# Kernel optimization log

Hardware: AMD Instinct MI355X
Metric: run time of the kernel (lower is better)

## Reference

```python
import jax, jax.numpy as jnp
import numpy as np

E = 8        # num experts
TOP = 2      # top-k
D = 1024     # emb_size


def setup_inputs() -> dict:
    key = jax.random.key(0)
    ks = jax.random.split(key, 8)
    s = 1.0 / np.sqrt(D)
    x = jax.random.normal(ks[0], (4, 2048, D), dtype=jnp.float32)
    Wg = jax.random.uniform(ks[1], (D, E), jnp.float32, -s, s)
    bg = jax.random.uniform(ks[2], (E,), jnp.float32, -s, s)
    W1 = jax.random.uniform(ks[3], (E, D, D), jnp.float32, -s, s)
    b1 = jax.random.uniform(ks[4], (E, D), jnp.float32, -s, s)
    W2 = jax.random.uniform(ks[5], (E, D, D), jnp.float32, -s, s)
    b2 = jax.random.uniform(ks[6], (E, D), jnp.float32, -s, s)
    return {"x": x, "Wg": Wg, "bg": bg, "W1": W1, "b1": b1, "W2": W2, "b2": b2}


def reference(x, Wg, bg, W1, b1, W2, b2):
    x_shape = x.shape
    xt = x.reshape(-1, x_shape[-1])                       # [N, D] tokens
    gate_prob = jax.nn.softmax(xt @ Wg + bg, axis=-1)     # [N, E]
    top_w, top_i = jax.lax.top_k(gate_prob, TOP)          # [N, TOP]
    top_w = jax.nn.softmax(top_w, axis=-1)                # renormalize over top-k
    N = xt.shape[0]
    # combine weights scattered into dense [N, E] (each token has TOP nonzeros)
    comb = jnp.zeros((N, E), xt.dtype).at[jnp.arange(N)[:, None], top_i].add(top_w)
    # per-expert 2-layer MLP applied to all tokens; masked-out tokens get 0 combine weight
    h = jax.nn.relu(jnp.einsum('nd,edf->enf', xt, W1) + b1[:, None, :])   # [E, N, D]
    ye = jnp.einsum('enf,efg->eng', h, W2) + b2[:, None, :]               # [E, N, D]
    y = jnp.einsum('ne,eng->ng', comb, ye)                                # [N, D]
    return y.reshape(x_shape), gate_prob
```

## Files before the change

kernel.cpp:

```cpp
#include <hip/hip_runtime.h>
#include <stdint.h>

#define TOKENS 8192
#define DIM    1024
#define NEXP   8
#define NASSIGN (TOKENS*2)
#define BK     64

#define C_ROW   16
#define C_TILE  25
#define C_TOTAL 34

#define WS_CTRL  0
#define WS_TOPE  1024
#define WS_TOPW  (WS_TOPE + NASSIGN*4)
#define WS_PTOK  (WS_TOPW + NASSIGN*4)
#define WS_AROW  (WS_PTOK + NASSIGN*4)
#define WS_XB    (WS_AROW + NASSIGN*4)
#define WS_W1T   (WS_XB  + (size_t)TOKENS*DIM*2)
#define WS_W2T   (WS_W1T + (size_t)NEXP*DIM*DIM*2)
#define WS_H     (WS_W2T + (size_t)NEXP*DIM*DIM*2)
#define WS_YE    WS_XB

#define WGLD (DIM + 4)

typedef __attribute__((ext_vector_type(8))) short short8;
typedef __attribute__((ext_vector_type(4))) float floatx4;

__device__ __forceinline__ uint32_t bfr(float f) {
  uint32_t v = __float_as_uint(f);
  return (v + 0x7FFFu + ((v >> 16) & 1u)) >> 16;
}
__device__ __forceinline__ float b2f(uint32_t u) { return __uint_as_float(u << 16); }

__device__ __forceinline__ void load_lds16(const void* g, void* l) {
  __builtin_amdgcn_global_load_lds(
      (const __attribute__((address_space(1))) uint32_t*)g,
      (__attribute__((address_space(3))) uint32_t*)l, 16, 0, 0);
}

__global__ __launch_bounds__(256) void prep_kernel(
    const float* __restrict__ x, const float* __restrict__ Wg,
    const float* __restrict__ bg, float* __restrict__ gate_out,
    int* __restrict__ top_e, float* __restrict__ top_w,
    uint16_t* __restrict__ xb,
    const float* __restrict__ W1, const float* __restrict__ W2,
    uint16_t* __restrict__ W1T, uint16_t* __restrict__ W2T) {
  __shared__ __align__(16) char smem[NEXP * WGLD * 4];
  int t = threadIdx.x;

  if (blockIdx.x >= 2048) {
    uint16_t (*tile)[68] = (uint16_t (*)[68])smem;
    int cb = blockIdx.x - 2048;
    int m  = cb >> 8;
    int d0 = ((cb >> 4) & 15) * 64, f0 = (cb & 15) * 64;
    const float* src = (m < 8) ? (W1 + (size_t)m*DIM*DIM) : (W2 + (size_t)(m-8)*DIM*DIM);
    uint16_t*    dst = (m < 8) ? (W1T + (size_t)m*DIM*DIM) : (W2T + (size_t)(m-8)*DIM*DIM);
    int col = t & 63, rb = (t >> 6) * 16;
    #pragma unroll
    for (int i = 0; i < 16; i++) {
      int dr = rb + i;
      tile[dr][col] = (uint16_t)bfr(src[(size_t)(d0+dr)*DIM + f0 + col]);
    }
    __syncthreads();
    int dg = t & 15, frb = t >> 4;
    #pragma unroll
    for (int i = 0; i < 4; i++) {
      int fr = frb + i * 16;
      uint32_t b0 = tile[dg*4+0][fr], b1 = tile[dg*4+1][fr];
      uint32_t b2 = tile[dg*4+2][fr], b3 = tile[dg*4+3][fr];
      uint2 v;
      v.x = b0 | (b1 << 16);
      v.y = b2 | (b3 << 16);
      *(uint2*)&dst[(size_t)(f0+fr)*DIM + d0 + dg*4] = v;
    }
    return;
  }

  float* wgs = (float*)smem;
  #pragma unroll
  for (int k = 0; k < 32; k++) {
    int i = k * 256 + t;
    float v = Wg[i];
    wgs[(i & 7) * WGLD + (i >> 3)] = v;
  }
  __syncthreads();

  int wave = t >> 6, lane = t & 63;
  int tok = blockIdx.x * 4 + wave;
  const float4* xr = (const float4*)(x + (size_t)tok * DIM);
  uint2* xw = (uint2*)(xb + (size_t)tok * DIM);

  float4 acc[NEXP];
  #pragma unroll
  for (int e = 0; e < NEXP; e++) acc[e] = make_float4(0.f, 0.f, 0.f, 0.f);

  #pragma unroll
  for (int c = 0; c < 4; c++) {
    float4 xv = xr[c * 64 + lane];
    uint2 o;
    o.x = bfr(xv.x) | (bfr(xv.y) << 16);
    o.y = bfr(xv.z) | (bfr(xv.w) << 16);
    xw[c * 64 + lane] = o;
    int d0 = (c * 64 + lane) * 4;
    #pragma unroll
    for (int e = 0; e < NEXP; e++) {
      float4 wv = *(const float4*)&wgs[e * WGLD + d0];
      acc[e].x = fmaf(xv.x, wv.x, acc[e].x);
      acc[e].y = fmaf(xv.y, wv.y, acc[e].y);
      acc[e].z = fmaf(xv.z, wv.z, acc[e].z);
      acc[e].w = fmaf(xv.w, wv.w, acc[e].w);
    }
  }
  float s[NEXP];
  #pragma unroll
  for (int e = 0; e < NEXP; e++) s[e] = (acc[e].x + acc[e].y) + (acc[e].z + acc[e].w);
  #pragma unroll
  for (int off = 32; off > 0; off >>= 1) {
    #pragma unroll
    for (int e = 0; e < NEXP; e++) s[e] += __shfl_xor(s[e], off);
  }
  if (lane == 0) {
    float lg[NEXP], p[NEXP];
    float mx = -1e30f;
    #pragma unroll
    for (int e = 0; e < NEXP; e++) { lg[e] = s[e] + bg[e]; mx = fmaxf(mx, lg[e]); }
    float sum = 0.f;
    #pragma unroll
    for (int e = 0; e < NEXP; e++) { p[e] = expf(lg[e] - mx); sum += p[e]; }
    float inv = 1.f / sum;
    #pragma unroll
    for (int e = 0; e < NEXP; e++) p[e] *= inv;
    float4* go = (float4*)(gate_out + (size_t)tok * NEXP);
    go[0] = make_float4(p[0], p[1], p[2], p[3]);
    go[1] = make_float4(p[4], p[5], p[6], p[7]);
    int i1 = 0;
    #pragma unroll
    for (int e = 1; e < NEXP; e++) if (p[e] > p[i1]) i1 = e;
    int i2 = (i1 == 0) ? 1 : 0;
    #pragma unroll
    for (int e = 0; e < NEXP; e++) if (e != i1 && p[e] > p[i2]) i2 = e;
    float ev = expf(p[i2] - p[i1]);
    float w1 = 1.f / (1.f + ev), w2 = ev / (1.f + ev);
    top_e[2*tok]   = i1; top_e[2*tok+1] = i2;
    top_w[2*tok]   = w1; top_w[2*tok+1] = w2;
  }
}

__global__ __launch_bounds__(1024) void route_kernel(
    const int* __restrict__ top_e, int* __restrict__ ctrl,
    int* __restrict__ ptok, int* __restrict__ arow) {
  __shared__ int sc[NEXP * 1024];
  __shared__ int scnt[NEXP];
  __shared__ int rowstart[NEXP];
  int t = threadIdx.x;
  int e_loc[16];
  int cnt[NEXP];
  #pragma unroll
  for (int e = 0; e < NEXP; e++) cnt[e] = 0;
  #pragma unroll
  for (int j = 0; j < 16; j++) {
    int e = top_e[t * 16 + j];
    e_loc[j] = e;
    cnt[e]++;
  }
  #pragma unroll
  for (int e = 0; e < NEXP; e++) sc[e * 1024 + t] = cnt[e];
  __syncthreads();
  int wave = t >> 6, lane = t & 63;
  if (wave < NEXP) {
    int running = 0;
    for (int chunk = 0; chunk < 16; chunk++) {
      int idx = wave * 1024 + chunk * 64 + lane;
      int v = sc[idx];
      int incl = v;
      #pragma unroll
      for (int off = 1; off < 64; off <<= 1) {
        int u = __shfl_up(incl, off);
        if (lane >= off) incl += u;
      }
      sc[idx] = running + incl - v;
      running += __shfl(incl, 63);
    }
    if (lane == 0) scnt[wave] = running;
  }
  __syncthreads();
  if (t == 0) {
    int rs = 0, ts = 0;
    for (int e = 0; e < NEXP; e++) {
      ctrl[C_ROW + e] = rs;
      ctrl[C_TILE + e] = ts;
      rowstart[e] = rs;
      int c = scnt[e];
      rs += c;
      ts += (c + 127) >> 7;
    }
    ctrl[C_ROW + NEXP] = rs;
    ctrl[C_TILE + NEXP] = ts;
    ctrl[C_TOTAL] = ts;
  }
  __syncthreads();
  int off[NEXP];
  #pragma unroll
  for (int e = 0; e < NEXP; e++) off[e] = rowstart[e] + sc[e * 1024 + t];
  #pragma unroll
  for (int j = 0; j < 16; j++) {
    int i = t * 16 + j;
    int e = e_loc[j];
    int pos = off[e]++;
    ptok[pos] = i >> 1;
    arow[i] = pos;
  }
}

__device__ __forceinline__ bool sched_map(const int* ctrl, int bid,
                                          int& mtile, int& n0) {
  int total = ctrl[C_TOTAL];
  int spx = (total + 7) >> 3;
  int xcd = bid & 7, j = bid >> 3;
  int slot = j >> 3;
  if (slot >= spx) return false;
  mtile = xcd * spx + slot;
  n0 = (j & 7) * 128;
  return mtile < total;
}

__global__ __launch_bounds__(256, 2) void gemm1_kernel(
    const uint16_t* __restrict__ xb, const uint16_t* __restrict__ w1t,
    const float* __restrict__ b1, const int* __restrict__ ctrl,
    const int* __restrict__ ptok, uint16_t* __restrict__ h) {
  __shared__ __align__(16) uint16_t As[128*BK];
  __shared__ __align__(16) uint16_t Bs[128*BK];
  int mtile, n0;
  if (!sched_map(ctrl, blockIdx.x, mtile, n0)) return;
  int e = 0;
  #pragma unroll
  for (int k = 1; k < NEXP; k++) if (mtile >= ctrl[C_TILE + k]) e = k;
  int row0 = ctrl[C_ROW + e] + (mtile - ctrl[C_TILE + e]) * 128;
  int rend = ctrl[C_ROW + e + 1];

  int t = threadIdx.x, lane = t & 63, w = t >> 6;
  const uint16_t* gA[4];
  const uint16_t* gB[4];
  #pragma unroll
  for (int i = 0; i < 4; i++) {
    int s = i * 256 + t;
    int row = s >> 3, cs = s & 7;
    int gc = cs ^ (row & 7);
    int ar = row0 + row; if (ar > NASSIGN-1) ar = NASSIGN-1;
    int tok = ptok[ar];
    gA[i] = xb  + (size_t)tok * DIM + gc*8;
    gB[i] = w1t + (size_t)e*DIM*DIM + (size_t)(n0 + row)*DIM + gc*8;
  }
  floatx4 acc[4][4];
  #pragma unroll
  for (int mi = 0; mi < 4; mi++)
    #pragma unroll
    for (int ni = 0; ni < 4; ni++) acc[mi][ni] = (floatx4)(0.f);

  int wm = w & 1, wn = w >> 1;
  int l15 = lane & 15, lq = lane >> 4;

  for (int kt = 0; kt < DIM/BK; kt++) {
    #pragma unroll
    for (int i = 0; i < 4; i++) {
      load_lds16(gA[i], &As[(i*256 + t) * 8]);
      load_lds16(gB[i], &Bs[(i*256 + t) * 8]);
      gA[i] += BK; gB[i] += BK;
    }
    __syncthreads();
    #pragma unroll
    for (int ks = 0; ks < 2; ks++) {
      short8 a[4], b[4];
      #pragma unroll
      for (int mi = 0; mi < 4; mi++) {
        int row = wm*64 + mi*16 + l15;
        int slot = (ks*4 + lq) ^ (row & 7);
        a[mi] = *(const short8*)&As[row*BK + slot*8];
      }
      #pragma unroll
      for (int ni = 0; ni < 4; ni++) {
        int row = wn*64 + ni*16 + l15;
        int slot = (ks*4 + lq) ^ (row & 7);
        b[ni] = *(const short8*)&Bs[row*BK + slot*8];
      }
      #pragma unroll
      for (int mi = 0; mi < 4; mi++)
        #pragma unroll
        for (int ni = 0; ni < 4; ni++)
          acc[mi][ni] = __builtin_amdgcn_mfma_f32_16x16x32_bf16(a[mi], b[ni], acc[mi][ni], 0, 0, 0);
    }
    __syncthreads();
  }
  #pragma unroll
  for (int mi = 0; mi < 4; mi++) {
    #pragma unroll
    for (int r = 0; r < 4; r++) {
      int rt = wm*64 + mi*16 + lq*4 + r;
      int ar = row0 + rt;
      if (ar < rend) {
        #pragma unroll
        for (int ni = 0; ni < 4; ni++) {
          int n = n0 + wn*64 + ni*16 + l15;
          float v = acc[mi][ni][r] + b1[e*DIM + n];
          v = fmaxf(v, 0.f);
          h[(size_t)ar*DIM + n] = (uint16_t)bfr(v);
        }
      }
    }
  }
}

__global__ __launch_bounds__(256, 2) void gemm2_kernel(
    const uint16_t* __restrict__ h, const uint16_t* __restrict__ w2t,
    const float* __restrict__ b2, const int* __restrict__ ctrl,
    uint16_t* __restrict__ yeb) {
  __shared__ __align__(16) uint16_t As[128*BK];
  __shared__ __align__(16) uint16_t Bs[128*BK];
  int mtile, n0;
  if (!sched_map(ctrl, blockIdx.x, mtile, n0)) return;
  int e = 0;
  #pragma unroll
  for (int k = 1; k < NEXP; k++) if (mtile >= ctrl[C_TILE + k]) e = k;
  int row0 = ctrl[C_ROW + e] + (mtile - ctrl[C_TILE + e]) * 128;
  int rend = ctrl[C_ROW + e + 1];

  int t = threadIdx.x, lane = t & 63, w = t >> 6;
  const uint16_t* gA[4];
  const uint16_t* gB[4];
  #pragma unroll
  for (int i = 0; i < 4; i++) {
    int s = i * 256 + t;
    int row = s >> 3, cs = s & 7;
    int gc = cs ^ (row & 7);
    int ar = row0 + row; if (ar > NASSIGN-1) ar = NASSIGN-1;
    gA[i] = h   + (size_t)ar * DIM + gc*8;
    gB[i] = w2t + (size_t)e*DIM*DIM + (size_t)(n0 + row)*DIM + gc*8;
  }
  floatx4 acc[4][4];
  #pragma unroll
  for (int mi = 0; mi < 4; mi++)
    #pragma unroll
    for (int ni = 0; ni < 4; ni++) acc[mi][ni] = (floatx4)(0.f);

  int wm = w & 1, wn = w >> 1;
  int l15 = lane & 15, lq = lane >> 4;

  for (int kt = 0; kt < DIM/BK; kt++) {
    #pragma unroll
    for (int i = 0; i < 4; i++) {
      load_lds16(gA[i], &As[(i*256 + t) * 8]);
      load_lds16(gB[i], &Bs[(i*256 + t) * 8]);
      gA[i] += BK; gB[i] += BK;
    }
    __syncthreads();
    #pragma unroll
    for (int ks = 0; ks < 2; ks++) {
      short8 a[4], b[4];
      #pragma unroll
      for (int mi = 0; mi < 4; mi++) {
        int row = wm*64 + mi*16 + l15;
        int slot = (ks*4 + lq) ^ (row & 7);
        a[mi] = *(const short8*)&As[row*BK + slot*8];
      }
      #pragma unroll
      for (int ni = 0; ni < 4; ni++) {
        int row = wn*64 + ni*16 + l15;
        int slot = (ks*4 + lq) ^ (row & 7);
        b[ni] = *(const short8*)&Bs[row*BK + slot*8];
      }
      #pragma unroll
      for (int mi = 0; mi < 4; mi++)
        #pragma unroll
        for (int ni = 0; ni < 4; ni++)
          acc[mi][ni] = __builtin_amdgcn_mfma_f32_16x16x32_bf16(a[mi], b[ni], acc[mi][ni], 0, 0, 0);
    }
    __syncthreads();
  }
  #pragma unroll
  for (int mi = 0; mi < 4; mi++) {
    #pragma unroll
    for (int r = 0; r < 4; r++) {
      int rt = wm*64 + mi*16 + lq*4 + r;
      int ar = row0 + rt;
      if (ar < rend) {
        #pragma unroll
        for (int ni = 0; ni < 4; ni++) {
          int n = n0 + wn*64 + ni*16 + l15;
          float v = acc[mi][ni][r] + b2[e*DIM + n];
          yeb[(size_t)ar*DIM + n] = (uint16_t)bfr(v);
        }
      }
    }
  }
}

__global__ __launch_bounds__(256) void combine_kernel(
    const uint16_t* __restrict__ yeb, const int* __restrict__ arow,
    const float* __restrict__ top_w, float* __restrict__ y) {
  int tok = blockIdx.x, t = threadIdx.x;
  int r0 = arow[2*tok], r1 = arow[2*tok+1];
  float w0 = top_w[2*tok], w1 = top_w[2*tok+1];
  const uint2* a = (const uint2*)(yeb + (size_t)r0 * DIM);
  const uint2* b = (const uint2*)(yeb + (size_t)r1 * DIM);
  uint2 av = a[t], bv = b[t];
  float4 o;
  o.x = w0 * b2f(av.x & 0xFFFFu) + w1 * b2f(bv.x & 0xFFFFu);
  o.y = w0 * b2f(av.x >> 16)     + w1 * b2f(bv.x >> 16);
  o.z = w0 * b2f(av.y & 0xFFFFu) + w1 * b2f(bv.y & 0xFFFFu);
  o.w = w0 * b2f(av.y >> 16)     + w1 * b2f(bv.y >> 16);
  ((float4*)(y + (size_t)tok * DIM))[t] = o;
}

extern "C" void kernel_launch(void* const* d_in, const int* in_sizes, int n_in,
                              void* d_out, int out_size, void* d_ws, size_t ws_size,
                              hipStream_t stream) {
  const float* x  = (const float*)d_in[0];
  const float* Wg = (const float*)d_in[1];
  const float* bg = (const float*)d_in[2];
  const float* W1 = (const float*)d_in[3];
  const float* b1 = (const float*)d_in[4];
  const float* W2 = (const float*)d_in[5];
  const float* b2 = (const float*)d_in[6];
  float* out = (float*)d_out;
  char* ws = (char*)d_ws;

  int*      ctrl = (int*)(ws + WS_CTRL);
  int*      tope = (int*)(ws + WS_TOPE);
  float*    topw = (float*)(ws + WS_TOPW);
  int*      ptok = (int*)(ws + WS_PTOK);
  int*      arow = (int*)(ws + WS_AROW);
  uint16_t* xb   = (uint16_t*)(ws + WS_XB);
  uint16_t* w1t  = (uint16_t*)(ws + WS_W1T);
  uint16_t* w2t  = (uint16_t*)(ws + WS_W2T);
  uint16_t* hbuf = (uint16_t*)(ws + WS_H);
  uint16_t* yeb  = (uint16_t*)(ws + WS_YE);

  prep_kernel<<<6144, 256, 0, stream>>>(x, Wg, bg, out + (size_t)TOKENS*DIM,
                                        tope, topw, xb, W1, W2, w1t, w2t);
  route_kernel<<<1, 1024, 0, stream>>>(tope, ctrl, ptok, arow);

  gemm1_kernel<<<136*8, 256, 0, stream>>>(xb, w1t, b1, ctrl, ptok, hbuf);
  gemm2_kernel<<<136*8, 256, 0, stream>>>(hbuf, w2t, b2, ctrl, yeb);
  combine_kernel<<<TOKENS, 256, 0, stream>>>(yeb, arow, topw, out);
}
```

Baseline: 269.7 us.

## Fuse combine into gemm2 via atomics and merge routing into weight prep

The gemm2 epilogue now scales each expert output row by its routing weight and atomically adds it into the zeroed fp32 output, which removes the bf16 intermediate buffer and the separate combine kernel. Gate computation is split into its own kernel, which also zeroes the output. Routing moves into block 0 of the weight transpose kernel, so the single-block route launch disappears and routing overlaps the transpose. The cost is float atomics on the output (2 adds per element) and non-deterministic summation order, and routing now runs on one 256-thread block in serial.

After: 329.7 us. +22.3%, slower.

```diff
diff --git a/kernel.cpp b/kernel.cpp
--- a/kernel.cpp
+++ b/kernel.cpp
@@ -15,12 +15,11 @@
 #define WS_TOPE  1024
 #define WS_TOPW  (WS_TOPE + NASSIGN*4)
 #define WS_PTOK  (WS_TOPW + NASSIGN*4)
-#define WS_AROW  (WS_PTOK + NASSIGN*4)
-#define WS_XB    (WS_AROW + NASSIGN*4)
+#define WS_PW    (WS_PTOK + NASSIGN*4)
+#define WS_XB    (WS_PW  + NASSIGN*4)
 #define WS_W1T   (WS_XB  + (size_t)TOKENS*DIM*2)
 #define WS_W2T   (WS_W1T + (size_t)NEXP*DIM*DIM*2)
 #define WS_H     (WS_W2T + (size_t)NEXP*DIM*DIM*2)
-#define WS_YE    WS_XB
 
 #define WGLD (DIM + 4)
 
@@ -39,19 +38,103 @@
       (__attribute__((address_space(3))) uint32_t*)l, 16, 0, 0);
 }
 
-__global__ __launch_bounds__(256) void prep_kernel(
+__global__ __launch_bounds__(256) void gate_kernel(
     const float* __restrict__ x, const float* __restrict__ Wg,
     const float* __restrict__ bg, float* __restrict__ gate_out,
     int* __restrict__ top_e, float* __restrict__ top_w,
-    uint16_t* __restrict__ xb,
+    uint16_t* __restrict__ xb, float* __restrict__ y) {
+  __shared__ __align__(16) float wgs[NEXP * WGLD];
+  int t = threadIdx.x;
+
+  {
+    float4 z = make_float4(0.f, 0.f, 0.f, 0.f);
+    float4* yz = (float4*)(y + (size_t)blockIdx.x * 4 * DIM);
+    #pragma unroll
+    for (int i = 0; i < 4; i++) yz[i * 256 + t] = z;
+  }
+
+  #pragma unroll
+  for (int k = 0; k < 32; k++) {
+    int i = k * 256 + t;
+    float v = Wg[i];
+    wgs[(i & 7) * WGLD + (i >> 3)] = v;
+  }
+  __syncthreads();
+
+  int wave = t >> 6, lane = t & 63;
+  int tok = blockIdx.x * 4 + wave;
+  const float4* xr = (const float4*)(x + (size_t)tok * DIM);
+  uint2* xw = (uint2*)(xb + (size_t)tok * DIM);
+
+  float4 acc[NEXP];
+  #pragma unroll
+  for (int e = 0; e < NEXP; e++) acc[e] = make_float4(0.f, 0.f, 0.f, 0.f);
+
+  #pragma unroll
+  for (int c = 0; c < 4; c++) {
+    float4 xv = xr[c * 64 + lane];
+    uint2 o;
+    o.x = bfr(xv.x) | (bfr(xv.y) << 16);
+    o.y = bfr(xv.z) | (bfr(xv.w) << 16);
+    xw[c * 64 + lane] = o;
+    int d0 = (c * 64 + lane) * 4;
+    #pragma unroll
+    for (int e = 0; e < NEXP; e++) {
+      float4 wv = *(const float4*)&wgs[e * WGLD + d0];
+      acc[e].x = fmaf(xv.x, wv.x, acc[e].x);
+      acc[e].y = fmaf(xv.y, wv.y, acc[e].y);
+      acc[e].z = fmaf(xv.z, wv.z, acc[e].z);
+      acc[e].w = fmaf(xv.w, wv.w, acc[e].w);
+    }
+  }
+  float s[NEXP];
+  #pragma unroll
+  for (int e = 0; e < NEXP; e++) s[e] = (acc[e].x + acc[e].y) + (acc[e].z + acc[e].w);
+  #pragma unroll
+  for (int off = 32; off > 0; off >>= 1) {
+    #pragma unroll
+    for (int e = 0; e < NEXP; e++) s[e] += __shfl_xor(s[e], off);
+  }
+  if (lane == 0) {
+    float lg[NEXP], p[NEXP];
+    float mx = -1e30f;
+    #pragma unroll
+    for (int e = 0; e < NEXP; e++) { lg[e] = s[e] + bg[e]; mx = fmaxf(mx, lg[e]); }
+    float sum = 0.f;
+    #pragma unroll
+    for (int e = 0; e < NEXP; e++) { p[e] = expf(lg[e] - mx); sum += p[e]; }
+    float inv = 1.f / sum;
+    #pragma unroll
+    for (int e = 0; e < NEXP; e++) p[e] *= inv;
+    float4* go = (float4*)(gate_out + (size_t)tok * NEXP);
+    go[0] = make_float4(p[0], p[1], p[2], p[3]);
+    go[1] = make_float4(p[4], p[5], p[6], p[7]);
+    int i1 = 0;
+    #pragma unroll
+    for (int e = 1; e < NEXP; e++) if (p[e] > p[i1]) i1 = e;
+    int i2 = (i1 == 0) ? 1 : 0;
+    #pragma unroll
+    for (int e = 0; e < NEXP; e++) if (e != i1 && p[e] > p[i2]) i2 = e;
+    float ev = expf(p[i2] - p[i1]);
+    float w1 = 1.f / (1.f + ev), w2 = ev / (1.f + ev);
+    top_e[2*tok]   = i1; top_e[2*tok+1] = i2;
+    top_w[2*tok]   = w1; top_w[2*tok+1] = w2;
+  }
+}
+
+__global__ __launch_bounds__(256) void prep2_kernel(
     const float* __restrict__ W1, const float* __restrict__ W2,
-    uint16_t* __restrict__ W1T, uint16_t* __restrict__ W2T) {
-  __shared__ __align__(16) char smem[NEXP * WGLD * 4];
+    uint16_t* __restrict__ W1T, uint16_t* __restrict__ W2T,
+    const int* __restrict__ top_e, const float* __restrict__ top_w,
+    int* __restrict__ ctrl, int* __restrict__ ptok, float* __restrict__ pw) {
+  __shared__ __align__(16) char smem[64 * 68 * 2];
+  __shared__ int scnt[NEXP];
+  __shared__ int rowstart[NEXP];
   int t = threadIdx.x;
 
-  if (blockIdx.x >= 2048) {
+  if (blockIdx.x != 0) {
     uint16_t (*tile)[68] = (uint16_t (*)[68])smem;
-    int cb = blockIdx.x - 2048;
+    int cb = blockIdx.x - 1;
     int m  = cb >> 8;
     int d0 = ((cb >> 4) & 15) * 64, f0 = (cb & 15) * 64;
     const float* src = (m < 8) ? (W1 + (size_t)m*DIM*DIM) : (W2 + (size_t)(m-8)*DIM*DIM);
@@ -77,101 +160,22 @@
     return;
   }
 
-  float* wgs = (float*)smem;
-  #pragma unroll
-  for (int k = 0; k < 32; k++) {
-    int i = k * 256 + t;
-    float v = Wg[i];
-    wgs[(i & 7) * WGLD + (i >> 3)] = v;
-  }
-  __syncthreads();
-
-  int wave = t >> 6, lane = t & 63;
-  int tok = blockIdx.x * 4 + wave;
-  const float4* xr = (const float4*)(x + (size_t)tok * DIM);
-  uint2* xw = (uint2*)(xb + (size_t)tok * DIM);
-
-  float4 acc[NEXP];
-  #pragma unroll
-  for (int e = 0; e < NEXP; e++) acc[e] = make_float4(0.f, 0.f, 0.f, 0.f);
-
-  #pragma unroll
-  for (int c = 0; c < 4; c++) {
-    float4 xv = xr[c * 64 + lane];
-    uint2 o;
-    o.x = bfr(xv.x) | (bfr(xv.y) << 16);
-    o.y = bfr(xv.z) | (bfr(xv.w) << 16);
-    xw[c * 64 + lane] = o;
-    int d0 = (c * 64 + lane) * 4;
-    #pragma unroll
-    for (int e = 0; e < NEXP; e++) {
-      float4 wv = *(const float4*)&wgs[e * WGLD + d0];
-      acc[e].x = fmaf(xv.x, wv.x, acc[e].x);
-      acc[e].y = fmaf(xv.y, wv.y, acc[e].y);
-      acc[e].z = fmaf(xv.z, wv.z, acc[e].z);
-      acc[e].w = fmaf(xv.w, wv.w, acc[e].w);
-    }
-  }
-  float s[NEXP];
-  #pragma unroll
-  for (int e = 0; e < NEXP; e++) s[e] = (acc[e].x + acc[e].y) + (acc[e].z + acc[e].w);
-  #pragma unroll
-  for (int off = 32; off > 0; off >>= 1) {
-    #pragma unroll
-    for (int e = 0; e < NEXP; e++) s[e] += __shfl_xor(s[e], off);
-  }
-  if (lane == 0) {
-    float lg[NEXP], p[NEXP];
-    float mx = -1e30f;
-    #pragma unroll
-    for (int e = 0; e < NEXP; e++) { lg[e] = s[e] + bg[e]; mx = fmaxf(mx, lg[e]); }
-    float sum = 0.f;
-    #pragma unroll
-    for (int e = 0; e < NEXP; e++) { p[e] = expf(lg[e] - mx); sum += p[e]; }
-    float inv = 1.f / sum;
-    #pragma unroll
-    for (int e = 0; e < NEXP; e++) p[e] *= inv;
-    float4* go = (float4*)(gate_out + (size_t)tok * NEXP);
-    go[0] = make_float4(p[0], p[1], p[2], p[3]);
-    go[1] = make_float4(p[4], p[5], p[6], p[7]);
-    int i1 = 0;
-    #pragma unroll
-    for (int e = 1; e < NEXP; e++) if (p[e] > p[i1]) i1 = e;
-    int i2 = (i1 == 0) ? 1 : 0;
-    #pragma unroll
-    for (int e = 0; e < NEXP; e++) if (e != i1 && p[e] > p[i2]) i2 = e;
-    float ev = expf(p[i2] - p[i1]);
-    float w1 = 1.f / (1.f + ev), w2 = ev / (1.f + ev);
-    top_e[2*tok]   = i1; top_e[2*tok+1] = i2;
-    top_w[2*tok]   = w1; top_w[2*tok+1] = w2;
-  }
-}
-
-__global__ __launch_bounds__(1024) void route_kernel(
-    const int* __restrict__ top_e, int* __restrict__ ctrl,
-    int* __restrict__ ptok, int* __restrict__ arow) {
-  __shared__ int sc[NEXP * 1024];
-  __shared__ int scnt[NEXP];
-  __shared__ int rowstart[NEXP];
-  int t = threadIdx.x;
-  int e_loc[16];
+  int* sc = (int*)smem;
   int cnt[NEXP];
   #pragma unroll
   for (int e = 0; e < NEXP; e++) cnt[e] = 0;
-  #pragma unroll
-  for (int j = 0; j < 16; j++) {
-    int e = top_e[t * 16 + j];
-    e_loc[j] = e;
+  for (int j = 0; j < 64; j++) {
+    int e = top_e[t * 64 + j];
     cnt[e]++;
   }
   #pragma unroll
-  for (int e = 0; e < NEXP; e++) sc[e * 1024 + t] = cnt[e];
+  for (int e = 0; e < NEXP; e++) sc[e * 256 + t] = cnt[e];
   __syncthreads();
   int wave = t >> 6, lane = t & 63;
-  if (wave < NEXP) {
+  for (int ee = wave; ee < NEXP; ee += 4) {
     int running = 0;
-    for (int chunk = 0; chunk < 16; chunk++) {
-      int idx = wave * 1024 + chunk * 64 + lane;
+    for (int chunk = 0; chunk < 4; chunk++) {
+      int idx = ee * 256 + chunk * 64 + lane;
       int v = sc[idx];
       int incl = v;
       #pragma unroll
@@ -182,7 +186,7 @@
       sc[idx] = running + incl - v;
       running += __shfl(incl, 63);
     }
-    if (lane == 0) scnt[wave] = running;
+    if (lane == 0) scnt[ee] = running;
   }
   __syncthreads();
   if (t == 0) {
@@ -202,14 +206,13 @@
   __syncthreads();
   int off[NEXP];
   #pragma unroll
-  for (int e = 0; e < NEXP; e++) off[e] = rowstart[e] + sc[e * 1024 + t];
-  #pragma unroll
-  for (int j = 0; j < 16; j++) {
-    int i = t * 16 + j;
-    int e = e_loc[j];
+  for (int e = 0; e < NEXP; e++) off[e] = rowstart[e] + sc[e * 256 + t];
+  for (int j = 0; j < 64; j++) {
+    int i = t * 64 + j;
+    int e = top_e[i];
     int pos = off[e]++;
     ptok[pos] = i >> 1;
-    arow[i] = pos;
+    pw[pos]   = top_w[i];
   }
 }
 
@@ -314,7 +317,8 @@
 __global__ __launch_bounds__(256, 2) void gemm2_kernel(
     const uint16_t* __restrict__ h, const uint16_t* __restrict__ w2t,
     const float* __restrict__ b2, const int* __restrict__ ctrl,
-    uint16_t* __restrict__ yeb) {
+    const int* __restrict__ ptok, const float* __restrict__ pw,
+    float* __restrict__ y) {
   __shared__ __align__(16) uint16_t As[128*BK];
   __shared__ __align__(16) uint16_t Bs[128*BK];
   int mtile, n0;
@@ -384,32 +388,18 @@
       int rt = wm*64 + mi*16 + lq*4 + r;
       int ar = row0 + rt;
       if (ar < rend) {
+        int tok   = ptok[ar];
+        float wgt = pw[ar];
+        float* yrow = y + (size_t)tok * DIM;
         #pragma unroll
         for (int ni = 0; ni < 4; ni++) {
           int n = n0 + wn*64 + ni*16 + l15;
           float v = acc[mi][ni][r] + b2[e*DIM + n];
-          yeb[(size_t)ar*DIM + n] = (uint16_t)bfr(v);
+          unsafeAtomicAdd(&yrow[n], wgt * v);
         }
       }
     }
   }
-}
-
-__global__ __launch_bounds__(256) void combine_kernel(
-    const uint16_t* __restrict__ yeb, const int* __restrict__ arow,
-    const float* __restrict__ top_w, float* __restrict__ y) {
-  int tok = blockIdx.x, t = threadIdx.x;
-  int r0 = arow[2*tok], r1 = arow[2*tok+1];
-  float w0 = top_w[2*tok], w1 = top_w[2*tok+1];
-  const uint2* a = (const uint2*)(yeb + (size_t)r0 * DIM);
-  const uint2* b = (const uint2*)(yeb + (size_t)r1 * DIM);
-  uint2 av = a[t], bv = b[t];
-  float4 o;
-  o.x = w0 * b2f(av.x & 0xFFFFu) + w1 * b2f(bv.x & 0xFFFFu);
-  o.y = w0 * b2f(av.x >> 16)     + w1 * b2f(bv.x >> 16);
-  o.z = w0 * b2f(av.y & 0xFFFFu) + w1 * b2f(bv.y & 0xFFFFu);
-  o.w = w0 * b2f(av.y >> 16)     + w1 * b2f(bv.y >> 16);
-  ((float4*)(y + (size_t)tok * DIM))[t] = o;
 }
 
 extern "C" void kernel_launch(void* const* d_in, const int* in_sizes, int n_in,
@@ -429,18 +419,16 @@
   int*      tope = (int*)(ws + WS_TOPE);
   float*    topw = (float*)(ws + WS_TOPW);
   int*      ptok = (int*)(ws + WS_PTOK);
-  int*      arow = (int*)(ws + WS_AROW);
+  float*    pww  = (float*)(ws + WS_PW);
   uint16_t* xb   = (uint16_t*)(ws + WS_XB);
   uint16_t* w1t  = (uint16_t*)(ws + WS_W1T);
   uint16_t* w2t  = (uint16_t*)(ws + WS_W2T);
   uint16_t* hbuf = (uint16_t*)(ws + WS_H);
-  uint16_t* yeb  = (uint16_t*)(ws + WS_YE);
-
-  prep_kernel<<<6144, 256, 0, stream>>>(x, Wg, bg, out + (size_t)TOKENS*DIM,
-                                        tope, topw, xb, W1, W2, w1t, w2t);
-  route_kernel<<<1, 1024, 0, stream>>>(tope, ctrl, ptok, arow);
-
+
+  gate_kernel<<<2048, 256, 0, stream>>>(x, Wg, bg, out + (size_t)TOKENS*DIM,
+                                        tope, topw, xb, out);
+  prep2_kernel<<<4097, 256, 0, stream>>>(W1, W2, w1t, w2t, tope, topw,
+                                         ctrl, ptok, pww);
   gemm1_kernel<<<136*8, 256, 0, stream>>>(xb, w1t, b1, ctrl, ptok, hbuf);
-  gemm2_kernel<<<136*8, 256, 0, stream>>>(hbuf, w2t, b2, ctrl, yeb);
-  combine_kernel<<<TOKENS, 256, 0, stream>>>(yeb, arow, topw, out);
-}
+  gemm2_kernel<<<136*8, 256, 0, stream>>>(hbuf, w2t, b2, ctrl, ptok, pww, out);
+}
```

## Overlap W2 bf16 transpose with gemm1 and widen combine loads

Applied to the files above, without the earlier changes.

Moves the W2 fp32-to-bf16 transpose out of the prep kernel and into extra trailing blocks of the gemm1 launch, so the conversion can run alongside the first expert GEMM instead of lengthening prep. The combine kernel now handles two tokens per block with 16-byte loads and two float4 stores per thread. The trade-off is that the conversion blocks compete with gemm1 for CUs and bandwidth, and their dispatch order relative to the GEMM blocks depends on the hardware scheduler.

Result: no change. 266.9 us, median of 2 (-1.0%).

```diff
diff --git a/kernel.cpp b/kernel.cpp
--- a/kernel.cpp
+++ b/kernel.cpp
@@ -6,6 +6,8 @@
 #define NEXP   8
 #define NASSIGN (TOKENS*2)
 #define BK     64
+#define NKT    (DIM/BK)
+#define G1BLK  1088
 
 #define C_ROW   16
 #define C_TILE  25
@@ -39,41 +41,44 @@
       (__attribute__((address_space(3))) uint32_t*)l, 16, 0, 0);
 }
 
+__device__ __forceinline__ void convw_tile(
+    const float* __restrict__ src, uint16_t* __restrict__ dst,
+    int d0, int f0, uint16_t (*tile)[68], int t) {
+  int col = t & 63, rb = (t >> 6) * 16;
+  #pragma unroll
+  for (int i = 0; i < 16; i++) {
+    int dr = rb + i;
+    tile[dr][col] = (uint16_t)bfr(src[(size_t)(d0+dr)*DIM + f0 + col]);
+  }
+  __syncthreads();
+  int dg = t & 15, frb = t >> 4;
+  #pragma unroll
+  for (int i = 0; i < 4; i++) {
+    int fr = frb + i * 16;
+    uint32_t c0 = tile[dg*4+0][fr], c1 = tile[dg*4+1][fr];
+    uint32_t c2 = tile[dg*4+2][fr], c3 = tile[dg*4+3][fr];
+    uint2 v;
+    v.x = c0 | (c1 << 16);
+    v.y = c2 | (c3 << 16);
+    *(uint2*)&dst[(size_t)(f0+fr)*DIM + d0 + dg*4] = v;
+  }
+}
+
 __global__ __launch_bounds__(256) void prep_kernel(
     const float* __restrict__ x, const float* __restrict__ Wg,
     const float* __restrict__ bg, float* __restrict__ gate_out,
     int* __restrict__ top_e, float* __restrict__ top_w,
     uint16_t* __restrict__ xb,
-    const float* __restrict__ W1, const float* __restrict__ W2,
-    uint16_t* __restrict__ W1T, uint16_t* __restrict__ W2T) {
+    const float* __restrict__ W1, uint16_t* __restrict__ W1T) {
   __shared__ __align__(16) char smem[NEXP * WGLD * 4];
   int t = threadIdx.x;
 
   if (blockIdx.x >= 2048) {
-    uint16_t (*tile)[68] = (uint16_t (*)[68])smem;
     int cb = blockIdx.x - 2048;
     int m  = cb >> 8;
     int d0 = ((cb >> 4) & 15) * 64, f0 = (cb & 15) * 64;
-    const float* src = (m < 8) ? (W1 + (size_t)m*DIM*DIM) : (W2 + (size_t)(m-8)*DIM*DIM);
-    uint16_t*    dst = (m < 8) ? (W1T + (size_t)m*DIM*DIM) : (W2T + (size_t)(m-8)*DIM*DIM);
-    int col = t & 63, rb = (t >> 6) * 16;
-    #pragma unroll
-    for (int i = 0; i < 16; i++) {
-      int dr = rb + i;
-      tile[dr][col] = (uint16_t)bfr(src[(size_t)(d0+dr)*DIM + f0 + col]);
-    }
-    __syncthreads();
-    int dg = t & 15, frb = t >> 4;
-    #pragma unroll
-    for (int i = 0; i < 4; i++) {
-      int fr = frb + i * 16;
-      uint32_t b0 = tile[dg*4+0][fr], b1 = tile[dg*4+1][fr];
-      uint32_t b2 = tile[dg*4+2][fr], b3 = tile[dg*4+3][fr];
-      uint2 v;
-      v.x = b0 | (b1 << 16);
-      v.y = b2 | (b3 << 16);
-      *(uint2*)&dst[(size_t)(f0+fr)*DIM + d0 + dg*4] = v;
-    }
+    convw_tile(W1 + (size_t)m*DIM*DIM, W1T + (size_t)m*DIM*DIM,
+               d0, f0, (uint16_t (*)[68])smem, t);
     return;
   }
 
@@ -228,9 +233,21 @@
 __global__ __launch_bounds__(256, 2) void gemm1_kernel(
     const uint16_t* __restrict__ xb, const uint16_t* __restrict__ w1t,
     const float* __restrict__ b1, const int* __restrict__ ctrl,
-    const int* __restrict__ ptok, uint16_t* __restrict__ h) {
+    const int* __restrict__ ptok, uint16_t* __restrict__ h,
+    const float* __restrict__ W2, uint16_t* __restrict__ w2t) {
   __shared__ __align__(16) uint16_t As[128*BK];
   __shared__ __align__(16) uint16_t Bs[128*BK];
+  int t = threadIdx.x;
+
+  if (blockIdx.x >= G1BLK) {
+    int cb = blockIdx.x - G1BLK;
+    int m  = cb >> 8;
+    int d0 = ((cb >> 4) & 15) * 64, f0 = (cb & 15) * 64;
+    convw_tile(W2 + (size_t)m*DIM*DIM, w2t + (size_t)m*DIM*DIM,
+               d0, f0, (uint16_t (*)[68])As, t);
+    return;
+  }
+
   int mtile, n0;
   if (!sched_map(ctrl, blockIdx.x, mtile, n0)) return;
   int e = 0;
@@ -239,7 +256,7 @@
   int row0 = ctrl[C_ROW + e] + (mtile - ctrl[C_TILE + e]) * 128;
   int rend = ctrl[C_ROW + e + 1];
 
-  int t = threadIdx.x, lane = t & 63, w = t >> 6;
+  int lane = t & 63, w = t >> 6;
   const uint16_t* gA[4];
   const uint16_t* gB[4];
   #pragma unroll
@@ -261,7 +278,7 @@
   int wm = w & 1, wn = w >> 1;
   int l15 = lane & 15, lq = lane >> 4;
 
-  for (int kt = 0; kt < DIM/BK; kt++) {
+  for (int kt = 0; kt < NKT; kt++) {
     #pragma unroll
     for (int i = 0; i < 4; i++) {
       load_lds16(gA[i], &As[(i*256 + t) * 8]);
@@ -346,7 +363,7 @@
   int wm = w & 1, wn = w >> 1;
   int l15 = lane & 15, lq = lane >> 4;
 
-  for (int kt = 0; kt < DIM/BK; kt++) {
+  for (int kt = 0; kt < NKT; kt++) {
     #pragma unroll
     for (int i = 0; i < 4; i++) {
       load_lds16(gA[i], &As[(i*256 + t) * 8]);
@@ -398,18 +415,26 @@
 __global__ __launch_bounds__(256) void combine_kernel(
     const uint16_t* __restrict__ yeb, const int* __restrict__ arow,
     const float* __restrict__ top_w, float* __restrict__ y) {
-  int tok = blockIdx.x, t = threadIdx.x;
+  int t = threadIdx.x;
+  int tok = blockIdx.x * 2 + (t >> 7);
+  int i = t & 127;
   int r0 = arow[2*tok], r1 = arow[2*tok+1];
   float w0 = top_w[2*tok], w1 = top_w[2*tok+1];
-  const uint2* a = (const uint2*)(yeb + (size_t)r0 * DIM);
-  const uint2* b = (const uint2*)(yeb + (size_t)r1 * DIM);
-  uint2 av = a[t], bv = b[t];
-  float4 o;
-  o.x = w0 * b2f(av.x & 0xFFFFu) + w1 * b2f(bv.x & 0xFFFFu);
-  o.y = w0 * b2f(av.x >> 16)     + w1 * b2f(bv.x >> 16);
-  o.z = w0 * b2f(av.y & 0xFFFFu) + w1 * b2f(bv.y & 0xFFFFu);
-  o.w = w0 * b2f(av.y >> 16)     + w1 * b2f(bv.y >> 16);
-  ((float4*)(y + (size_t)tok * DIM))[t] = o;
+  const uint4* a = (const uint4*)(yeb + (size_t)r0 * DIM);
+  const uint4* b = (const uint4*)(yeb + (size_t)r1 * DIM);
+  uint4 av = a[i], bv = b[i];
+  float4* yo = (float4*)(y + (size_t)tok * DIM + i * 8);
+  float4 o0, o1;
+  o0.x = w0 * b2f(av.x & 0xFFFFu) + w1 * b2f(bv.x & 0xFFFFu);
+  o0.y = w0 * b2f(av.x >> 16)     + w1 * b2f(bv.x >> 16);
+  o0.z = w0 * b2f(av.y & 0xFFFFu) + w1 * b2f(bv.y & 0xFFFFu);
+  o0.w = w0 * b2f(av.y >> 16)     + w1 * b2f(bv.y >> 16);
+  o1.x = w0 * b2f(av.z & 0xFFFFu) + w1 * b2f(bv.z & 0xFFFFu);
+  o1.y = w0 * b2f(av.z >> 16)     + w1 * b2f(bv.z >> 16);
+  o1.z = w0 * b2f(av.w & 0xFFFFu) + w1 * b2f(bv.w & 0xFFFFu);
+  o1.w = w0 * b2f(av.w >> 16)     + w1 * b2f(bv.w >> 16);
+  yo[0] = o0;
+  yo[1] = o1;
 }
 
 extern "C" void kernel_launch(void* const* d_in, const int* in_sizes, int n_in,
@@ -436,11 +461,11 @@
   uint16_t* hbuf = (uint16_t*)(ws + WS_H);
   uint16_t* yeb  = (uint16_t*)(ws + WS_YE);
 
-  prep_kernel<<<6144, 256, 0, stream>>>(x, Wg, bg, out + (size_t)TOKENS*DIM,
-                                        tope, topw, xb, W1, W2, w1t, w2t);
+  prep_kernel<<<4096, 256, 0, stream>>>(x, Wg, bg, out + (size_t)TOKENS*DIM,
+                                        tope, topw, xb, W1, w1t);
   route_kernel<<<1, 1024, 0, stream>>>(tope, ctrl, ptok, arow);
-
-  gemm1_kernel<<<136*8, 256, 0, stream>>>(xb, w1t, b1, ctrl, ptok, hbuf);
+  gemm1_kernel<<<G1BLK + 2048, 256, 0, stream>>>(xb, w1t, b1, ctrl, ptok, hbuf,
+                                                 W2, w2t);
   gemm2_kernel<<<136*8, 256, 0, stream>>>(hbuf, w2t, b2, ctrl, yeb);
-  combine_kernel<<<TOKENS, 256, 0, stream>>>(yeb, arow, topw, out);
-}
+  combine_kernel<<<TOKENS/2, 256, 0, stream>>>(yeb, arow, topw, out);
+}
```
